# Kernel tuning notes

Hardware: AMD Instinct MI355X
Metric: run time of the kernel (lower is better)

## Reference

```python
import jax, jax.numpy as jnp
import numpy as np

DIM = 32
NUM_FEATURES = 11
N_NODES = 65536
N_EDGES = 262144


def setup_inputs() -> dict:
    key = jax.random.key(0)
    ks = jax.random.split(key, 16)
    s = 0.05
    return {
        "x": jax.random.normal(ks[0], (N_NODES, NUM_FEATURES), dtype=jnp.float32),
        "edge_index": jax.random.randint(ks[1], (2, N_EDGES), 0, N_NODES, dtype=jnp.int32),
        "edge_attr": jax.random.uniform(ks[2], (N_EDGES, 1), dtype=jnp.float32),
        # lin0: num_features -> dim
        "lin0_w": jax.random.normal(ks[3], (NUM_FEATURES, DIM), dtype=jnp.float32) * s,
        "lin0_b": jnp.zeros((DIM,), dtype=jnp.float32),
        # edge MLP: 1 -> 64 -> dim*dim
        "nn_w1": jax.random.normal(ks[4], (1, 64), dtype=jnp.float32) * s,
        "nn_b1": jnp.zeros((64,), dtype=jnp.float32),
        "nn_w2": jax.random.normal(ks[5], (64, DIM * DIM), dtype=jnp.float32) * s,
        "nn_b2": jnp.zeros((DIM * DIM,), dtype=jnp.float32),
        # NNConv root weight + bias
        "root": jax.random.normal(ks[6], (DIM, DIM), dtype=jnp.float32) * s,
        "conv_bias": jnp.zeros((DIM,), dtype=jnp.float32),
        # lin2: dim -> 1
        "lin2_w": jax.random.normal(ks[7], (DIM, 1), dtype=jnp.float32) * s,
        "lin2_b": jnp.zeros((1,), dtype=jnp.float32),
    }


def reference(x, edge_index, edge_attr, lin0_w, lin0_b, nn_w1, nn_b1, nn_w2, nn_b2,
              root, conv_bias, lin2_w, lin2_b):
    N = x.shape[0]
    src, dst = edge_index[0], edge_index[1]

    # out = relu(lin0(x))
    h = jax.nn.relu(x @ lin0_w + lin0_b)  # [N, dim]

    # Per-edge weight matrices from the edge MLP (edge_attr is loop-invariant).
    ew = jax.nn.relu(edge_attr @ nn_w1 + nn_b1) @ nn_w2 + nn_b2  # [E, dim*dim]
    W = ew.reshape(-1, DIM, DIM)  # [E, in, out]

    # In-degree counts for mean aggregation (isolated nodes -> 0, like PyG scatter mean).
    counts = jax.ops.segment_sum(jnp.ones_like(dst, dtype=h.dtype), dst, num_segments=N)
    inv_counts = jnp.where(counts > 0, 1.0 / jnp.maximum(counts, 1.0), 0.0)[:, None]

    def nnconv(h):
        msg = jnp.einsum('ei,eio->eo', h[src], W)  # gather + per-edge matvec
        agg = jax.ops.segment_sum(msg, dst, num_segments=N) * inv_counts  # scatter-mean
        return agg + h @ root + conv_bias

    for _ in range(8):
        h = h + jax.nn.relu(nnconv(h))

    g = jnp.mean(h, axis=0)  # [dim]
    return (g @ lin2_w + lin2_b).reshape(-1)  # [1]
```

## Files before the change

### kernel.cpp

```cpp
#include <hip/hip_runtime.h>

#define N_NODES 65536
#define N_EDGES 262144

typedef _Float16 f16;
typedef __attribute__((ext_vector_type(8))) _Float16 f16x8;
typedef __attribute__((ext_vector_type(4))) float f32x4;


__global__ void vmat_kernel(const float* __restrict__ w1, const float* __restrict__ b1,
                            const float* __restrict__ w2, const float* __restrict__ b2,
                            f16* __restrict__ Bv16, f16* __restrict__ BvE,
                            f16* __restrict__ Bb16, f16* __restrict__ BbE,
                            int* __restrict__ flag) {
    int jj = blockIdx.x * 256 + threadIdx.x;
    float v = 0.0f, c0 = 0.0f;
#pragma unroll
    for (int k = 0; k < 64; ++k) {
        float w = w1[k];
        if (w > 0.0f) {
            float wv = w2[k * 1024 + jj];
            v += w * wv;
            c0 += b1[k] * wv;
        }
    }
    float bt = c0 + b2[jj];
    int i = jj >> 5, o = jj & 31;
    f16 v16 = (f16)v;
    Bv16[o * 32 + i] = v16;
    BvE[o * 32 + i] = (f16)(v - (float)v16);
    f16 t16 = (f16)bt;
    Bb16[o * 32 + i] = t16;
    BbE[o * 32 + i] = (f16)(bt - (float)t16);
    if (bt != 0.0f) atomicOr(flag, 1);
}

__global__ void prep_root_kernel(const float* __restrict__ root,
                                 f16* __restrict__ Br16, f16* __restrict__ BrE) {
    int jj = blockIdx.x * 256 + threadIdx.x;
    int i = jj >> 5, o = jj & 31;
    float r = root[jj];
    f16 r16 = (f16)r;
    Br16[o * 32 + i] = r16;
    BrE[o * 32 + i] = (f16)(r - (float)r16);
}

__global__ void lin0_kernel(const float* __restrict__ x, const float* __restrict__ w,
                            const float* __restrict__ b, f16* __restrict__ h16,
                            f16* __restrict__ herr) {
    int idx = blockIdx.x * 256 + threadIdx.x;
    int n = idx >> 5, j = idx & 31;
    float acc = b[j];
#pragma unroll
    for (int i = 0; i < 11; ++i) acc += x[n * 11 + i] * w[i * 32 + j];
    float hv = fmaxf(acc, 0.0f);
    f16 q = (f16)hv;
    h16[idx] = q;
    herr[idx] = (f16)(hv - (float)q);
}

__global__ void hist_kernel(const int* __restrict__ dst, int* __restrict__ counts) {
    int e = blockIdx.x * 256 + threadIdx.x;
    if (e < N_EDGES) atomicAdd(&counts[dst[e]], 1);
}

__global__ void scan_kernel(const int* __restrict__ counts, int* __restrict__ offs) {
    __shared__ int part[1024];
    int t = threadIdx.x;
    int base = t * 64;
    int s = 0;
    for (int i = 0; i < 64; ++i) s += counts[base + i];
    part[t] = s;
    __syncthreads();
    for (int off = 1; off < 1024; off <<= 1) {
        int v = part[t];
        int add = (t >= off) ? part[t - off] : 0;
        __syncthreads();
        part[t] = v + add;
        __syncthreads();
    }
    int run = (t == 0) ? 0 : part[t - 1];
    for (int i = 0; i < 64; ++i) { offs[base + i] = run; run += counts[base + i]; }
    if (t == 1023) offs[N_NODES] = run;
}

__global__ void inv_kernel(const int* __restrict__ counts, float* __restrict__ inv) {
    int n = blockIdx.x * 256 + threadIdx.x;
    int c = counts[n];
    inv[n] = (c > 0) ? (1.0f / (float)c) : 0.0f;
}

__global__ void fill_kernel(const int* __restrict__ src, const int* __restrict__ dst,
                            const float* __restrict__ attr, const int* __restrict__ offs,
                            const float* __restrict__ inv, int* __restrict__ cursor,
                            int2* __restrict__ edgeRec, float* __restrict__ qc) {
    int e = blockIdx.x * 256 + threadIdx.x;
    if (e >= N_EDGES) return;
    int d = dst[e];
    int p = offs[d] + atomicAdd(&cursor[d], 1);
    edgeRec[p] = make_int2((src[e] & 0xffff) | ((d & 3) << 16), __float_as_int(attr[e] * inv[d]));
    qc[p] = inv[d];
}

__global__ __launch_bounds__(256, 4) void iter4_kernel(
    const f16* __restrict__ h16in, const f16* __restrict__ herrin,
    f16* __restrict__ h16out, f16* __restrict__ herrout,
    const int* __restrict__ offs, const int2* __restrict__ edgeRec,
    const float* __restrict__ qc,
    const f16* __restrict__ Bv16, const f16* __restrict__ BvE,
    const f16* __restrict__ Br16, const f16* __restrict__ BrE,
    const f16* __restrict__ Bb16, const f16* __restrict__ BbE,
    const float* __restrict__ bias, const int* __restrict__ flag) {
    __shared__ float aS[4][16][36];
    __shared__ float bS[4][16][36];
    int t = threadIdx.x;
    int w = t >> 6, lane = t & 63;
    int j = lane & 31, half = lane >> 5;
    int fn = lane & 15, fk = (lane >> 4) * 8;
    bool useB = (flag[0] != 0);
    int g16 = (blockIdx.x * 4 + w) * 16;

    const f16x8 bv0  = *(const f16x8*)&Bv16[fn * 32 + fk];
    const f16x8 bv1  = *(const f16x8*)&Bv16[(fn + 16) * 32 + fk];
    const f16x8 bvE0 = *(const f16x8*)&BvE[fn * 32 + fk];
    const f16x8 bvE1 = *(const f16x8*)&BvE[(fn + 16) * 32 + fk];
    const f16x8 br0  = *(const f16x8*)&Br16[fn * 32 + fk];
    const f16x8 br1  = *(const f16x8*)&Br16[(fn + 16) * 32 + fk];
    const f16x8 brE0 = *(const f16x8*)&BrE[fn * 32 + fk];
    const f16x8 brE1 = *(const f16x8*)&BrE[(fn + 16) * 32 + fk];

    for (int rr = 0; rr < 4; ++rr) {
        int m0 = g16 + rr * 4;
        int pb = offs[m0], pe = offs[m0 + 4];
        float a0 = 0.f, a1 = 0.f, a2 = 0.f, a3 = 0.f;
        for (int p = pb + half * 8; p < pe; p += 16) {
            int2 rc[8]; float g[8];
#pragma unroll
            for (int k = 0; k < 8; ++k) rc[k] = edgeRec[min(p + k, pe - 1)];
#pragma unroll
            for (int k = 0; k < 8; ++k) g[k] = (float)h16in[(rc[k].x & 0xffff) * 32 + j];
#pragma unroll
            for (int k = 0; k < 8; ++k) {
                float c = (p + k < pe) ? __int_as_float(rc[k].y) : 0.0f;
                int dl = (rc[k].x >> 16) & 3;
                a0 = fmaf((dl == 0) ? c : 0.0f, g[k], a0);
                a1 = fmaf((dl == 1) ? c : 0.0f, g[k], a1);
                a2 = fmaf((dl == 2) ? c : 0.0f, g[k], a2);
                a3 = fmaf((dl == 3) ? c : 0.0f, g[k], a3);
            }
        }
        a0 += __shfl_xor(a0, 32); a1 += __shfl_xor(a1, 32);
        a2 += __shfl_xor(a2, 32); a3 += __shfl_xor(a3, 32);
        aS[w][rr * 4 + 0][j] = a0; aS[w][rr * 4 + 1][j] = a1;
        aS[w][rr * 4 + 2][j] = a2; aS[w][rr * 4 + 3][j] = a3;
        if (useB) {
            float q0 = 0.f, q1 = 0.f, q2 = 0.f, q3 = 0.f;
            for (int p = pb + half * 8; p < pe; p += 16) {
                for (int k = 0; k < 8; ++k) {
                    int idx = min(p + k, pe - 1);
                    int2 r = edgeRec[idx];
                    float g = (float)h16in[(r.x & 0xffff) * 32 + j];
                    float c = (p + k < pe) ? qc[idx] : 0.0f;
                    int dl = (r.x >> 16) & 3;
                    q0 += (dl == 0) ? c * g : 0.f; q1 += (dl == 1) ? c * g : 0.f;
                    q2 += (dl == 2) ? c * g : 0.f; q3 += (dl == 3) ? c * g : 0.f;
                }
            }
            q0 += __shfl_xor(q0, 32); q1 += __shfl_xor(q1, 32);
            q2 += __shfl_xor(q2, 32); q3 += __shfl_xor(q3, 32);
            bS[w][rr * 4 + 0][j] = q0; bS[w][rr * 4 + 1][j] = q1;
            bS[w][rr * 4 + 2][j] = q2; bS[w][rr * 4 + 3][j] = q3;
        }
    }

    f16x8 a16, aE;
#pragma unroll
    for (int i = 0; i < 8; ++i) {
        float av = aS[w][fn][fk + i];
        f16 lo = (f16)av;
        a16[i] = lo;
        aE[i] = (f16)(av - (float)lo);
    }
    f16x8 hf  = *(const f16x8*)&h16in[(g16 + fn) * 32 + fk];
    f16x8 hfe = *(const f16x8*)&herrin[(g16 + fn) * 32 + fk];
    f32x4 c0 = {0.f, 0.f, 0.f, 0.f}, c1 = {0.f, 0.f, 0.f, 0.f};
    c0 = __builtin_amdgcn_mfma_f32_16x16x32_f16(a16, bv0,  c0, 0, 0, 0);
    c0 = __builtin_amdgcn_mfma_f32_16x16x32_f16(a16, bvE0, c0, 0, 0, 0);
    c0 = __builtin_amdgcn_mfma_f32_16x16x32_f16(aE,  bv0,  c0, 0, 0, 0);
    c0 = __builtin_amdgcn_mfma_f32_16x16x32_f16(hf,  br0,  c0, 0, 0, 0);
    c0 = __builtin_amdgcn_mfma_f32_16x16x32_f16(hf,  brE0, c0, 0, 0, 0);
    c0 = __builtin_amdgcn_mfma_f32_16x16x32_f16(hfe, br0,  c0, 0, 0, 0);
    c1 = __builtin_amdgcn_mfma_f32_16x16x32_f16(a16, bv1,  c1, 0, 0, 0);
    c1 = __builtin_amdgcn_mfma_f32_16x16x32_f16(a16, bvE1, c1, 0, 0, 0);
    c1 = __builtin_amdgcn_mfma_f32_16x16x32_f16(aE,  bv1,  c1, 0, 0, 0);
    c1 = __builtin_amdgcn_mfma_f32_16x16x32_f16(hf,  br1,  c1, 0, 0, 0);
    c1 = __builtin_amdgcn_mfma_f32_16x16x32_f16(hf,  brE1, c1, 0, 0, 0);
    c1 = __builtin_amdgcn_mfma_f32_16x16x32_f16(hfe, br1,  c1, 0, 0, 0);
    if (useB) {
        f16x8 ab16, abE;
#pragma unroll
        for (int i = 0; i < 8; ++i) {
            float av = bS[w][fn][fk + i];
            f16 lo = (f16)av;
            ab16[i] = lo;
            abE[i] = (f16)(av - (float)lo);
        }
        f16x8 bb0  = *(const f16x8*)&Bb16[fn * 32 + fk];
        f16x8 bb1  = *(const f16x8*)&Bb16[(fn + 16) * 32 + fk];
        f16x8 bbE0 = *(const f16x8*)&BbE[fn * 32 + fk];
        f16x8 bbE1 = *(const f16x8*)&BbE[(fn + 16) * 32 + fk];
        c0 = __builtin_amdgcn_mfma_f32_16x16x32_f16(ab16, bb0,  c0, 0, 0, 0);
        c0 = __builtin_amdgcn_mfma_f32_16x16x32_f16(ab16, bbE0, c0, 0, 0, 0);
        c0 = __builtin_amdgcn_mfma_f32_16x16x32_f16(abE,  bb0,  c0, 0, 0, 0);
        c1 = __builtin_amdgcn_mfma_f32_16x16x32_f16(ab16, bb1,  c1, 0, 0, 0);
        c1 = __builtin_amdgcn_mfma_f32_16x16x32_f16(ab16, bbE1, c1, 0, 0, 0);
        c1 = __builtin_amdgcn_mfma_f32_16x16x32_f16(abE,  bb1,  c1, 0, 0, 0);
    }

    float bj0 = bias[fn], bj1 = bias[fn + 16];
    int rbase = (lane >> 4) * 4;
#pragma unroll
    for (int r = 0; r < 4; ++r) {
        int n = g16 + rbase + r;
        float u0 = c0[r] + bj0, u1 = c1[r] + bj1;
        float hv0 = (float)h16in[n * 32 + fn] + (float)herrin[n * 32 + fn];
        float hv1 = (float)h16in[n * 32 + fn + 16] + (float)herrin[n * 32 + fn + 16];
        float hn0 = hv0 + fmaxf(u0, 0.0f);
        float hn1 = hv1 + fmaxf(u1, 0.0f);
        f16 p0 = (f16)hn0, p1 = (f16)hn1;
        h16out[n * 32 + fn] = p0;
        herrout[n * 32 + fn] = (f16)(hn0 - (float)p0);
        h16out[n * 32 + fn + 16] = p1;
        herrout[n * 32 + fn + 16] = (f16)(hn1 - (float)p1);
    }
}


__global__ void reduce_kernel(const f16* __restrict__ h16, const f16* __restrict__ herr,
                              float* __restrict__ gacc) {
    int j = threadIdx.x & 31, g = threadIdx.x >> 5;
    float s = 0.0f;
    int node0 = blockIdx.x * 128;
    for (int n = node0 + g; n < node0 + 128; n += 8)
        s += (float)h16[n * 32 + j] + (float)herr[n * 32 + j];
    __shared__ float red[8][32];
    red[g][j] = s;
    __syncthreads();
    if (g == 0) {
        float tt = 0.0f;
        for (int k = 0; k < 8; ++k) tt += red[k][j];
        atomicAdd(&gacc[j], tt);
    }
}

__global__ void out_kernel(const float* __restrict__ gacc, const float* __restrict__ w,
                           const float* __restrict__ b, float* __restrict__ out) {
    if (threadIdx.x == 0) {
        float acc = 0.0f;
        for (int j = 0; j < 32; ++j) acc += gacc[j] * w[j];
        out[0] = acc * (1.0f / (float)N_NODES) + b[0];
    }
}


extern "C" void kernel_launch(void* const* d_in, const int* in_sizes, int n_in,
                              void* d_out, int out_size, void* d_ws, size_t ws_size,
                              hipStream_t stream) {
    (void)in_sizes; (void)n_in; (void)out_size; (void)ws_size;
    const float* x        = (const float*)d_in[0];
    const int*   eidx     = (const int*)d_in[1];
    const float* eattr    = (const float*)d_in[2];
    const float* lin0_w   = (const float*)d_in[3];
    const float* lin0_b   = (const float*)d_in[4];
    const float* nn_w1    = (const float*)d_in[5];
    const float* nn_b1    = (const float*)d_in[6];
    const float* nn_w2    = (const float*)d_in[7];
    const float* nn_b2    = (const float*)d_in[8];
    const float* root     = (const float*)d_in[9];
    const float* conv_b   = (const float*)d_in[10];
    const float* lin2_w   = (const float*)d_in[11];
    const float* lin2_b   = (const float*)d_in[12];
    float* out = (float*)d_out;

    const int* src = eidx;
    const int* dst = eidx + N_EDGES;

    char* ws = (char*)d_ws;
    size_t off = 0;
    f16* h16A = (f16*)(ws + off); off += (size_t)N_NODES * 32 * 2;
    f16* h16B = (f16*)(ws + off); off += (size_t)N_NODES * 32 * 2;
    f16* heA  = (f16*)(ws + off); off += (size_t)N_NODES * 32 * 2;
    f16* heB  = (f16*)(ws + off); off += (size_t)N_NODES * 32 * 2;
    f16* Bv16 = (f16*)(ws + off); off += 2048;
    f16* BvE  = (f16*)(ws + off); off += 2048;
    f16* Br16 = (f16*)(ws + off); off += 2048;
    f16* BrE  = (f16*)(ws + off); off += 2048;
    f16* Bb16 = (f16*)(ws + off); off += 2048;
    f16* BbE  = (f16*)(ws + off); off += 2048;
    float* inv  = (float*)(ws + off); off += (size_t)N_NODES * 4;
    int*   offs = (int*)(ws + off);   off += 262400;
    int2*  edgeRec = (int2*)(ws + off); off += (size_t)N_EDGES * 8;
    float* qc   = (float*)(ws + off); off += (size_t)N_EDGES * 4;
    char*  zbase  = ws + off;
    int*   counts = (int*)zbase;
    int*   cursor = (int*)(zbase + (size_t)N_NODES * 4);
    float* gacc   = (float*)(zbase + (size_t)N_NODES * 8);
    int*   flag   = (int*)(zbase + (size_t)N_NODES * 8 + 128);
    size_t zsize  = (size_t)N_NODES * 8 + 256;

    hipMemsetAsync(zbase, 0, zsize, stream);

    vmat_kernel<<<4, 256, 0, stream>>>(nn_w1, nn_b1, nn_w2, nn_b2, Bv16, BvE, Bb16, BbE, flag);
    prep_root_kernel<<<4, 256, 0, stream>>>(root, Br16, BrE);
    lin0_kernel<<<(N_NODES * 32) / 256, 256, 0, stream>>>(x, lin0_w, lin0_b, h16A, heA);
    hist_kernel<<<N_EDGES / 256, 256, 0, stream>>>(dst, counts);
    scan_kernel<<<1, 1024, 0, stream>>>(counts, offs);
    inv_kernel<<<N_NODES / 256, 256, 0, stream>>>(counts, inv);
    fill_kernel<<<N_EDGES / 256, 256, 0, stream>>>(src, dst, eattr, offs, inv, cursor, edgeRec, qc);

    f16* hbuf[2] = {h16A, h16B};
    f16* ebuf[2] = {heA, heB};
    for (int it = 0; it < 8; ++it) {
        iter4_kernel<<<N_NODES / 64, 256, 0, stream>>>(
            hbuf[it & 1], ebuf[it & 1], hbuf[(it + 1) & 1], ebuf[(it + 1) & 1],
            offs, edgeRec, qc, Bv16, BvE, Br16, BrE, Bb16, BbE, conv_b, flag);
    }

    reduce_kernel<<<N_NODES / 128, 256, 0, stream>>>(h16A, heA, gacc);
    out_kernel<<<1, 64, 0, stream>>>(gacc, lin2_w, lin2_b, out);
}
```

Baseline: 251.2 us.

## Drop fp16 error-compensation buffer for node state and prefetch edge records

Removes the split-fp16 residual (herr) for node features, so h is stored as a single fp16 value. This halves node-state memory traffic per iteration and drops two MFMAs per tile. The aggregation loop now prefetches the next batch of edge records while the current gathers are processed, and the B-fragment loads are moved after the loop to lower register pressure. The cost is lower precision: h accumulates a rounding error across 8 residual iterations, which may fall outside tolerance.

```diff
diff --git a/kernel.cpp b/kernel.cpp
--- a/kernel.cpp
+++ b/kernel.cpp
@@ -46,17 +46,13 @@
 }
 
 __global__ void lin0_kernel(const float* __restrict__ x, const float* __restrict__ w,
-                            const float* __restrict__ b, f16* __restrict__ h16,
-                            f16* __restrict__ herr) {
+                            const float* __restrict__ b, f16* __restrict__ h16) {
     int idx = blockIdx.x * 256 + threadIdx.x;
     int n = idx >> 5, j = idx & 31;
     float acc = b[j];
 #pragma unroll
     for (int i = 0; i < 11; ++i) acc += x[n * 11 + i] * w[i * 32 + j];
-    float hv = fmaxf(acc, 0.0f);
-    f16 q = (f16)hv;
-    h16[idx] = q;
-    herr[idx] = (f16)(hv - (float)q);
+    h16[idx] = (f16)fmaxf(acc, 0.0f);
 }
 
 __global__ void hist_kernel(const int* __restrict__ dst, int* __restrict__ counts) {
@@ -102,9 +98,8 @@
     qc[p] = inv[d];
 }
 
-__global__ __launch_bounds__(256, 4) void iter4_kernel(
-    const f16* __restrict__ h16in, const f16* __restrict__ herrin,
-    f16* __restrict__ h16out, f16* __restrict__ herrout,
+__global__ __launch_bounds__(256, 4) void iter5_kernel(
+    const f16* __restrict__ h16in, f16* __restrict__ h16out,
     const int* __restrict__ offs, const int2* __restrict__ edgeRec,
     const float* __restrict__ qc,
     const f16* __restrict__ Bv16, const f16* __restrict__ BvE,
@@ -120,6 +115,65 @@
     bool useB = (flag[0] != 0);
     int g16 = (blockIdx.x * 4 + w) * 16;
 
+    for (int rr = 0; rr < 4; ++rr) {
+        int m0 = g16 + rr * 4;
+        int pb = offs[m0], pe = offs[m0 + 4];
+        float a0 = 0.f, a1 = 0.f, a2 = 0.f, a3 = 0.f;
+        int p = pb + half * 8;
+        if (p < pe) {
+            int2 rc[8];
+#pragma unroll
+            for (int k = 0; k < 8; ++k) rc[k] = edgeRec[min(p + k, pe - 1)];
+            while (true) {
+                float g[8];
+#pragma unroll
+                for (int k = 0; k < 8; ++k) g[k] = (float)h16in[(rc[k].x & 0xffff) * 32 + j];
+                int pn = p + 16;
+                bool more = (pn < pe);
+                int2 rn[8];
+                if (more) {
+#pragma unroll
+                    for (int k = 0; k < 8; ++k) rn[k] = edgeRec[min(pn + k, pe - 1)];
+                }
+#pragma unroll
+                for (int k = 0; k < 8; ++k) {
+                    float c = (p + k < pe) ? __int_as_float(rc[k].y) : 0.0f;
+                    int dl = (rc[k].x >> 16) & 3;
+                    a0 = fmaf((dl == 0) ? c : 0.0f, g[k], a0);
+                    a1 = fmaf((dl == 1) ? c : 0.0f, g[k], a1);
+                    a2 = fmaf((dl == 2) ? c : 0.0f, g[k], a2);
+                    a3 = fmaf((dl == 3) ? c : 0.0f, g[k], a3);
+                }
+                if (!more) break;
+#pragma unroll
+                for (int k = 0; k < 8; ++k) rc[k] = rn[k];
+                p = pn;
+            }
+        }
+        a0 += __shfl_xor(a0, 32); a1 += __shfl_xor(a1, 32);
+        a2 += __shfl_xor(a2, 32); a3 += __shfl_xor(a3, 32);
+        aS[w][rr * 4 + 0][j] = a0; aS[w][rr * 4 + 1][j] = a1;
+        aS[w][rr * 4 + 2][j] = a2; aS[w][rr * 4 + 3][j] = a3;
+        if (useB) {
+            float q0 = 0.f, q1 = 0.f, q2 = 0.f, q3 = 0.f;
+            for (int pp = pb + half * 8; pp < pe; pp += 16) {
+                for (int k = 0; k < 8; ++k) {
+                    int idx = min(pp + k, pe - 1);
+                    int2 r = edgeRec[idx];
+                    float gg = (float)h16in[(r.x & 0xffff) * 32 + j];
+                    float c = (pp + k < pe) ? qc[idx] : 0.0f;
+                    int dl = (r.x >> 16) & 3;
+                    q0 += (dl == 0) ? c * gg : 0.f; q1 += (dl == 1) ? c * gg : 0.f;
+                    q2 += (dl == 2) ? c * gg : 0.f; q3 += (dl == 3) ? c * gg : 0.f;
+                }
+            }
+            q0 += __shfl_xor(q0, 32); q1 += __shfl_xor(q1, 32);
+            q2 += __shfl_xor(q2, 32); q3 += __shfl_xor(q3, 32);
+            bS[w][rr * 4 + 0][j] = q0; bS[w][rr * 4 + 1][j] = q1;
+            bS[w][rr * 4 + 2][j] = q2; bS[w][rr * 4 + 3][j] = q3;
+        }
+    }
+
     const f16x8 bv0  = *(const f16x8*)&Bv16[fn * 32 + fk];
     const f16x8 bv1  = *(const f16x8*)&Bv16[(fn + 16) * 32 + fk];
     const f16x8 bvE0 = *(const f16x8*)&BvE[fn * 32 + fk];
@@ -128,51 +182,6 @@
     const f16x8 br1  = *(const f16x8*)&Br16[(fn + 16) * 32 + fk];
     const f16x8 brE0 = *(const f16x8*)&BrE[fn * 32 + fk];
     const f16x8 brE1 = *(const f16x8*)&BrE[(fn + 16) * 32 + fk];
-
-    for (int rr = 0; rr < 4; ++rr) {
-        int m0 = g16 + rr * 4;
-        int pb = offs[m0], pe = offs[m0 + 4];
-        float a0 = 0.f, a1 = 0.f, a2 = 0.f, a3 = 0.f;
-        for (int p = pb + half * 8; p < pe; p += 16) {
-            int2 rc[8]; float g[8];
-#pragma unroll
-            for (int k = 0; k < 8; ++k) rc[k] = edgeRec[min(p + k, pe - 1)];
-#pragma unroll
-            for (int k = 0; k < 8; ++k) g[k] = (float)h16in[(rc[k].x & 0xffff) * 32 + j];
-#pragma unroll
-            for (int k = 0; k < 8; ++k) {
-                float c = (p + k < pe) ? __int_as_float(rc[k].y) : 0.0f;
-                int dl = (rc[k].x >> 16) & 3;
-                a0 = fmaf((dl == 0) ? c : 0.0f, g[k], a0);
-                a1 = fmaf((dl == 1) ? c : 0.0f, g[k], a1);
-                a2 = fmaf((dl == 2) ? c : 0.0f, g[k], a2);
-                a3 = fmaf((dl == 3) ? c : 0.0f, g[k], a3);
-            }
-        }
-        a0 += __shfl_xor(a0, 32); a1 += __shfl_xor(a1, 32);
-        a2 += __shfl_xor(a2, 32); a3 += __shfl_xor(a3, 32);
-        aS[w][rr * 4 + 0][j] = a0; aS[w][rr * 4 + 1][j] = a1;
-        aS[w][rr * 4 + 2][j] = a2; aS[w][rr * 4 + 3][j] = a3;
-        if (useB) {
-            float q0 = 0.f, q1 = 0.f, q2 = 0.f, q3 = 0.f;
-            for (int p = pb + half * 8; p < pe; p += 16) {
-                for (int k = 0; k < 8; ++k) {
-                    int idx = min(p + k, pe - 1);
-                    int2 r = edgeRec[idx];
-                    float g = (float)h16in[(r.x & 0xffff) * 32 + j];
-                    float c = (p + k < pe) ? qc[idx] : 0.0f;
-                    int dl = (r.x >> 16) & 3;
-                    q0 += (dl == 0) ? c * g : 0.f; q1 += (dl == 1) ? c * g : 0.f;
-                    q2 += (dl == 2) ? c * g : 0.f; q3 += (dl == 3) ? c * g : 0.f;
-                }
-            }
-            q0 += __shfl_xor(q0, 32); q1 += __shfl_xor(q1, 32);
-            q2 += __shfl_xor(q2, 32); q3 += __shfl_xor(q3, 32);
-            bS[w][rr * 4 + 0][j] = q0; bS[w][rr * 4 + 1][j] = q1;
-            bS[w][rr * 4 + 2][j] = q2; bS[w][rr * 4 + 3][j] = q3;
-        }
-    }
-
     f16x8 a16, aE;
 #pragma unroll
     for (int i = 0; i < 8; ++i) {
@@ -181,21 +190,18 @@
         a16[i] = lo;
         aE[i] = (f16)(av - (float)lo);
     }
-    f16x8 hf  = *(const f16x8*)&h16in[(g16 + fn) * 32 + fk];
-    f16x8 hfe = *(const f16x8*)&herrin[(g16 + fn) * 32 + fk];
+    f16x8 hf = *(const f16x8*)&h16in[(g16 + fn) * 32 + fk];
     f32x4 c0 = {0.f, 0.f, 0.f, 0.f}, c1 = {0.f, 0.f, 0.f, 0.f};
     c0 = __builtin_amdgcn_mfma_f32_16x16x32_f16(a16, bv0,  c0, 0, 0, 0);
     c0 = __builtin_amdgcn_mfma_f32_16x16x32_f16(a16, bvE0, c0, 0, 0, 0);
     c0 = __builtin_amdgcn_mfma_f32_16x16x32_f16(aE,  bv0,  c0, 0, 0, 0);
     c0 = __builtin_amdgcn_mfma_f32_16x16x32_f16(hf,  br0,  c0, 0, 0, 0);
     c0 = __builtin_amdgcn_mfma_f32_16x16x32_f16(hf,  brE0, c0, 0, 0, 0);
-    c0 = __builtin_amdgcn_mfma_f32_16x16x32_f16(hfe, br0,  c0, 0, 0, 0);
     c1 = __builtin_amdgcn_mfma_f32_16x16x32_f16(a16, bv1,  c1, 0, 0, 0);
     c1 = __builtin_amdgcn_mfma_f32_16x16x32_f16(a16, bvE1, c1, 0, 0, 0);
     c1 = __builtin_amdgcn_mfma_f32_16x16x32_f16(aE,  bv1,  c1, 0, 0, 0);
     c1 = __builtin_amdgcn_mfma_f32_16x16x32_f16(hf,  br1,  c1, 0, 0, 0);
     c1 = __builtin_amdgcn_mfma_f32_16x16x32_f16(hf,  brE1, c1, 0, 0, 0);
-    c1 = __builtin_amdgcn_mfma_f32_16x16x32_f16(hfe, br1,  c1, 0, 0, 0);
     if (useB) {
         f16x8 ab16, abE;
 #pragma unroll
@@ -222,27 +228,20 @@
 #pragma unroll
     for (int r = 0; r < 4; ++r) {
         int n = g16 + rbase + r;
-        float u0 = c0[r] + bj0, u1 = c1[r] + bj1;
-        float hv0 = (float)h16in[n * 32 + fn] + (float)herrin[n * 32 + fn];
-        float hv1 = (float)h16in[n * 32 + fn + 16] + (float)herrin[n * 32 + fn + 16];
-        float hn0 = hv0 + fmaxf(u0, 0.0f);
-        float hn1 = hv1 + fmaxf(u1, 0.0f);
-        f16 p0 = (f16)hn0, p1 = (f16)hn1;
-        h16out[n * 32 + fn] = p0;
-        herrout[n * 32 + fn] = (f16)(hn0 - (float)p0);
-        h16out[n * 32 + fn + 16] = p1;
-        herrout[n * 32 + fn + 16] = (f16)(hn1 - (float)p1);
-    }
-}
-
-
-__global__ void reduce_kernel(const f16* __restrict__ h16, const f16* __restrict__ herr,
-                              float* __restrict__ gacc) {
+        float hn0 = (float)h16in[n * 32 + fn] + fmaxf(c0[r] + bj0, 0.0f);
+        float hn1 = (float)h16in[n * 32 + fn + 16] + fmaxf(c1[r] + bj1, 0.0f);
+        h16out[n * 32 + fn] = (f16)hn0;
+        h16out[n * 32 + fn + 16] = (f16)hn1;
+    }
+}
+
+
+__global__ void reduce_kernel(const f16* __restrict__ h16, float* __restrict__ gacc) {
     int j = threadIdx.x & 31, g = threadIdx.x >> 5;
     float s = 0.0f;
     int node0 = blockIdx.x * 128;
     for (int n = node0 + g; n < node0 + 128; n += 8)
-        s += (float)h16[n * 32 + j] + (float)herr[n * 32 + j];
+        s += (float)h16[n * 32 + j];
     __shared__ float red[8][32];
     red[g][j] = s;
     __syncthreads();
@@ -289,8 +288,6 @@
     size_t off = 0;
     f16* h16A = (f16*)(ws + off); off += (size_t)N_NODES * 32 * 2;
     f16* h16B = (f16*)(ws + off); off += (size_t)N_NODES * 32 * 2;
-    f16* heA  = (f16*)(ws + off); off += (size_t)N_NODES * 32 * 2;
-    f16* heB  = (f16*)(ws + off); off += (size_t)N_NODES * 32 * 2;
     f16* Bv16 = (f16*)(ws + off); off += 2048;
     f16* BvE  = (f16*)(ws + off); off += 2048;
     f16* Br16 = (f16*)(ws + off); off += 2048;
@@ -312,20 +309,19 @@
 
     vmat_kernel<<<4, 256, 0, stream>>>(nn_w1, nn_b1, nn_w2, nn_b2, Bv16, BvE, Bb16, BbE, flag);
     prep_root_kernel<<<4, 256, 0, stream>>>(root, Br16, BrE);
-    lin0_kernel<<<(N_NODES * 32) / 256, 256, 0, stream>>>(x, lin0_w, lin0_b, h16A, heA);
+    lin0_kernel<<<(N_NODES * 32) / 256, 256, 0, stream>>>(x, lin0_w, lin0_b, h16A);
     hist_kernel<<<N_EDGES / 256, 256, 0, stream>>>(dst, counts);
     scan_kernel<<<1, 1024, 0, stream>>>(counts, offs);
     inv_kernel<<<N_NODES / 256, 256, 0, stream>>>(counts, inv);
     fill_kernel<<<N_EDGES / 256, 256, 0, stream>>>(src, dst, eattr, offs, inv, cursor, edgeRec, qc);
 
     f16* hbuf[2] = {h16A, h16B};
-    f16* ebuf[2] = {heA, heB};
     for (int it = 0; it < 8; ++it) {
-        iter4_kernel<<<N_NODES / 64, 256, 0, stream>>>(
-            hbuf[it & 1], ebuf[it & 1], hbuf[(it + 1) & 1], ebuf[(it + 1) & 1],
+        iter5_kernel<<<N_NODES / 64, 256, 0, stream>>>(
+            hbuf[it & 1], hbuf[(it + 1) & 1],
             offs, edgeRec, qc, Bv16, BvE, Br16, BrE, Bb16, BbE, conv_b, flag);
     }
 
-    reduce_kernel<<<N_NODES / 128, 256, 0, stream>>>(h16A, heA, gacc);
+    reduce_kernel<<<N_NODES / 128, 256, 0, stream>>>(h16A, gacc);
     out_kernel<<<1, 64, 0, stream>>>(gacc, lin2_w, lin2_b, out);
 }
```

Result: faster. 241.0 us (-4.1%).
